# Kernel optimization log

Measured on AMD Instinct MI355X. Metric: run time of the kernel, lower is better.

The kernel has to match this reference:

```python
import jax, jax.numpy as jnp
import numpy as np

H = 64
FF = 128
V = 64
B = 256
L = 4096


def setup_inputs() -> dict:
    key = jax.random.key(0)
    ks = jax.random.split(key, 16)
    s = 0.02
    inp = {
        'seq':   jax.random.randint(ks[0], (B, L), 0, V, dtype=jnp.int32),
        'embed': jax.random.normal(ks[1], (V, H), jnp.float32) * s,
        'W1':    jax.random.normal(ks[2], (H, FF), jnp.float32) * s,
        'b1':    jnp.zeros((FF,), jnp.float32),
        'W2':    jax.random.normal(ks[3], (FF, H), jnp.float32) * s,
        'b2':    jnp.zeros((H,), jnp.float32),
        'gamma': jnp.ones((H,), jnp.float32),
        'beta':  jnp.zeros((H,), jnp.float32),
        'Wk':    jax.random.normal(ks[4], (H, H), jnp.float32) * s,
        'Wv':    jax.random.normal(ks[5], (H, H), jnp.float32) * s,
        'Wq':    jax.random.normal(ks[6], (H, H), jnp.float32) * s,
        'Wr':    jax.random.normal(ks[7], (H, H), jnp.float32) * s,
        'br':    jnp.zeros((H,), jnp.float32),
        'Wo':    jax.random.normal(ks[8], (H, V), jnp.float32) * s,
        'bo':    jnp.zeros((V,), jnp.float32),
    }
    return inp


def reference(seq, embed, W1, b1, W2, b2, gamma, beta, Wk, Wv, Wq, Wr, br, Wo, bo):
    # token embedding + FFN residual + LayerNorm
    h = embed[seq]                                            # (B,L,H)
    x = h + jnp.maximum(h @ W1 + b1, 0.0) @ W2 + b2
    mu = x.mean(-1, keepdims=True)
    var = ((x - mu) ** 2).mean(-1, keepdims=True)
    hn = (x - mu) * jax.lax.rsqrt(var + 1e-5) * gamma + beta  # (B,L,H)

    # precompute all keys/values for steps 0..L-2 (batched GEMMs)
    hk = hn[:, :-1]                                           # (B,L-1,H)
    k = hk @ Wk
    v = hk @ Wv
    kn = k / jnp.maximum(jnp.linalg.norm(k, axis=-1, keepdims=True), 1e-12)

    # sequential delta-rule fast-weight update via scan over time
    def step(M, kv):
        kt, vt = kv                                           # (B,H), (B,H)
        vp = jnp.einsum('bij,bj->bi', M, kt)                  # predicted value
        M = M + jnp.einsum('bi,bj->bij', vt - vp, kt)         # rank-1 delta write
        return M, None

    M0 = jnp.zeros((hn.shape[0], H, H), hn.dtype)
    M, _ = jax.lax.scan(step, M0, (kn.transpose(1, 0, 2), v.transpose(1, 0, 2)))

    # read out with last-position query
    q = hn[:, -1] @ Wq                                        # (B,H)
    r = jnp.einsum('bij,bj->bi', M, q) @ Wr + br
    return r @ Wo + bo                                        # (B,V)
```

## Files before the change

### kernel.cpp

```cpp
#include <hip/hip_runtime.h>
#include <hip/hip_bf16.h>

#define H_ 64
#define FF_ 128
#define V_ 64
#define B_ 256
#define L_ 4096

typedef __attribute__((ext_vector_type(2))) float f32x2;
typedef __attribute__((ext_vector_type(4))) int i32x4;

__device__ __forceinline__ float wsum64(float x) {
  #pragma unroll
  for (int m = 32; m; m >>= 1) x += __shfl_xor(x, m, 64);
  return x;
}
__device__ __forceinline__ float readlane_f(float x, int lane) {
  return __int_as_float(__builtin_amdgcn_readlane(__float_as_int(x), lane));
}

__global__ __launch_bounds__(64) void build_tables(
    const float* __restrict__ embed, const float* __restrict__ W1,
    const float* __restrict__ b1, const float* __restrict__ W2,
    const float* __restrict__ b2, const float* __restrict__ gamma,
    const float* __restrict__ beta, const float* __restrict__ Wk,
    const float* __restrict__ Wv, const float* __restrict__ Wq,
    float2* __restrict__ kv_table, float* __restrict__ q_table)
{
  const int tok = blockIdx.x;
  const int l = threadIdx.x;
  __shared__ float sh_h[H_];
  __shared__ float sh_a[FF_];
  __shared__ float sh_n[H_];

  float h = embed[tok * H_ + l];
  sh_h[l] = h;
  __syncthreads();

  float a0 = b1[l], a1 = b1[l + 64];
  #pragma unroll 8
  for (int j = 0; j < H_; ++j) {
    float hj = sh_h[j];
    a0 = fmaf(hj, W1[j * FF_ + l], a0);
    a1 = fmaf(hj, W1[j * FF_ + l + 64], a1);
  }
  sh_a[l]      = fmaxf(a0, 0.f);
  sh_a[l + 64] = fmaxf(a1, 0.f);
  __syncthreads();

  float x = h + b2[l];
  #pragma unroll 8
  for (int f = 0; f < FF_; ++f) x = fmaf(sh_a[f], W2[f * H_ + l], x);

  float mu = wsum64(x) * (1.0f / 64.0f);
  float d = x - mu;
  float var = wsum64(d * d) * (1.0f / 64.0f);
  float hn = d * rsqrtf(var + 1e-5f) * gamma[l] + beta[l];
  sh_n[l] = hn;
  __syncthreads();

  float k = 0.f, v = 0.f, q = 0.f;
  #pragma unroll 8
  for (int i = 0; i < H_; ++i) {
    float hi = sh_n[i];
    k = fmaf(hi, Wk[i * H_ + l], k);
    v = fmaf(hi, Wv[i * H_ + l], v);
    q = fmaf(hi, Wq[i * H_ + l], q);
  }
  float n2 = wsum64(k * k);
  float kn = k / fmaxf(sqrtf(n2), 1e-12f);
  kv_table[tok * H_ + l] = make_float2(kn, v);
  q_table[tok * H_ + l] = q;
}

__global__ __launch_bounds__(64) void build_gram(
    const float2* __restrict__ kv_table, float* __restrict__ gram)
{
  const int arow = blockIdx.x;
  const int j = threadIdx.x;
  float s = 0.f;
  #pragma unroll 8
  for (int i = 0; i < H_; ++i)
    s = fmaf(kv_table[arow * H_ + i].x, kv_table[j * H_ + i].x, s);
  gram[arow * H_ + j] = s;
}

#define DS64(dst, addr)  asm volatile("ds_read_b64 %0, %1"  : "=v"(dst) : "v"(addr))
#define DS128(dst, addr) asm volatile("ds_read_b128 %0, %1" : "=v"(dst) : "v"(addr))
#define LGKM(n) do { asm volatile("s_waitcnt lgkmcnt(" #n ")" ::: "memory"); \
                     __builtin_amdgcn_sched_barrier(0); } while (0)

#define PREP(S) do { \
  ss##S##0 = __builtin_amdgcn_readfirstlane(tk##S.w); \
  ss##S##1 = __builtin_amdgcn_readfirstlane(tk##S.z); \
  ss##S##2 = __builtin_amdgcn_readfirstlane(tk##S.y); \
  ss##S##3 = __builtin_amdgcn_readfirstlane(tk##S.x); \
  DS64(rb##S##0, gv_base + (unsigned)(ss##S##0) * 512u); \
  DS64(rb##S##1, gv_base + (unsigned)(ss##S##1) * 512u); \
  DS64(rb##S##2, gv_base + (unsigned)(ss##S##2) * 512u); \
  DS64(rb##S##3, gv_base + (unsigned)(ss##S##3) * 512u); \
} while (0)

#define TOKLD(S) do { \
  DS128(tk##S, atok); \
  atok = (atok >= tok_base + 16u) ? (atok - 16u) : tok_base; \
} while (0)

#define EXEC(S) do { \
  float d_; \
  d_ = readlane_f(a, ss##S##0); a = fmaf(-d_, (rb##S##0).x, a); r = fmaf(d_, (rb##S##0).y, r); \
  d_ = readlane_f(a, ss##S##1); a = fmaf(-d_, (rb##S##1).x, a); r = fmaf(d_, (rb##S##1).y, r); \
  d_ = readlane_f(a, ss##S##2); a = fmaf(-d_, (rb##S##2).x, a); r = fmaf(d_, (rb##S##2).y, r); \
  d_ = readlane_f(a, ss##S##3); a = fmaf(-d_, (rb##S##3).x, a); r = fmaf(d_, (rb##S##3).y, r); \
} while (0)

#define PHASE(EP, PP) do { \
  LGKM(5); \
  PREP(PP); \
  TOKLD(EP); \
  LGKM(11); \
  EXEC(EP); \
} while (0)

__global__ __launch_bounds__(64) void scan_kernel(
    const int* __restrict__ seq, const float2* __restrict__ kv_table,
    const float* __restrict__ q_table, const float* __restrict__ gram,
    const float* __restrict__ Wr, const float* __restrict__ br,
    const float* __restrict__ Wo, const float* __restrict__ bo,
    float* __restrict__ out)
{
  const int b = blockIdx.x, l = threadIdx.x;
  __shared__ __align__(16) int stok[L_];
  __shared__ float kn_s[64 * 65];
  __shared__ __align__(8) float2 gv_s[64 * 64];
  __shared__ float qs[64], sh_r[64], sh_rr[64];

  {
    const int4* src = reinterpret_cast<const int4*>(seq + b * L_);
    int4* dst = reinterpret_cast<int4*>(stok);
    for (int i = l; i < 1024; i += 64) dst[i] = src[i];
  }
  for (int idx = l * 2; idx < 4096; idx += 128) {
    float4 kv2 = *reinterpret_cast<const float4*>(&kv_table[idx]);
    float2 g2 = *reinterpret_cast<const float2*>(&gram[idx]);
    int row = idx >> 6, col = idx & 63;
    kn_s[row * 65 + col] = kv2.x;
    kn_s[row * 65 + col + 1] = kv2.z;
    gv_s[idx] = make_float2(g2.x, kv2.y);
    gv_s[idx + 1] = make_float2(g2.y, kv2.w);
  }
  __syncthreads();

  const int tq = stok[L_ - 1];
  qs[l] = q_table[tq * 64 + l];
  __syncthreads();

  float a = 0.f;
  #pragma unroll 8
  for (int i = 0; i < 64; ++i) a = fmaf(kn_s[l * 65 + i], qs[i], a);
  float r = 0.f;

  const float2* gvl = gv_s + l;
  #pragma unroll
  for (int t = 4094; t >= 4092; --t) {
    int s0 = __builtin_amdgcn_readfirstlane(stok[t]);
    float2 g = gvl[s0 * 64];
    float c0 = readlane_f(a, s0);
    a = fmaf(-c0, g.x, a);
    r = fmaf(c0, g.y, r);
  }

  unsigned tok_base = (unsigned)(size_t)stok;
  unsigned gv_base  = (unsigned)(size_t)gv_s + (unsigned)l * 8u;
  i32x4 tk0, tk1, tk2, tk3;
  f32x2 rb00, rb01, rb02, rb03, rb10, rb11, rb12, rb13,
        rb20, rb21, rb22, rb23, rb30, rb31, rb32, rb33;
  int ss00, ss01, ss02, ss03, ss10, ss11, ss12, ss13,
      ss20, ss21, ss22, ss23, ss30, ss31, ss32, ss33;

  DS128(tk0, tok_base + 16352u);
  DS128(tk1, tok_base + 16336u);
  LGKM(0);
  PREP(0);
  DS128(tk2, tok_base + 16320u);
  PREP(1);
  DS128(tk3, tok_base + 16304u);
  unsigned atok = tok_base + 16288u;

  #pragma unroll 1
  for (int it = 0; it < 255; ++it) {
    PHASE(0, 2);
    PHASE(1, 3);
    PHASE(2, 0);
    PHASE(3, 1);
  }
  PHASE(0, 2);
  PHASE(1, 3);
  PHASE(2, 0);
  LGKM(0);

  sh_r[l] = r;
  __syncthreads();
  float rr = br[l];
  #pragma unroll 8
  for (int i = 0; i < 64; ++i) rr = fmaf(sh_r[i], Wr[i * 64 + l], rr);
  sh_rr[l] = rr;
  __syncthreads();
  float o = bo[l];
  #pragma unroll 8
  for (int j = 0; j < 64; ++j) o = fmaf(sh_rr[j], Wo[j * 64 + l], o);
  out[b * V_ + l] = o;
}

extern "C" void kernel_launch(void* const* d_in, const int* in_sizes, int n_in,
                              void* d_out, int out_size, void* d_ws, size_t ws_size,
                              hipStream_t stream) {
  const int*   seq   = (const int*)  d_in[0];
  const float* embed = (const float*)d_in[1];
  const float* W1    = (const float*)d_in[2];
  const float* b1    = (const float*)d_in[3];
  const float* W2    = (const float*)d_in[4];
  const float* b2    = (const float*)d_in[5];
  const float* gamma = (const float*)d_in[6];
  const float* beta  = (const float*)d_in[7];
  const float* Wk    = (const float*)d_in[8];
  const float* Wv    = (const float*)d_in[9];
  const float* Wq    = (const float*)d_in[10];
  const float* Wr    = (const float*)d_in[11];
  const float* br    = (const float*)d_in[12];
  const float* Wo    = (const float*)d_in[13];
  const float* bo    = (const float*)d_in[14];
  float* out = (float*)d_out;

  float2* kv_table = (float2*)d_ws;
  float*  q_table  = (float*)((char*)d_ws + 32 * 1024);
  float*  gram     = (float*)((char*)d_ws + 48 * 1024);

  build_tables<<<V_, 64, 0, stream>>>(embed, W1, b1, W2, b2, gamma, beta,
                                      Wk, Wv, Wq, kv_table, q_table);
  build_gram<<<V_, 64, 0, stream>>>(kv_table, gram);
  scan_kernel<<<B_, 64, 0, stream>>>(seq, kv_table, q_table, gram,
                                     Wr, br, Wo, bo, out);
}
```

Before: 204.7 us.

## Precompute per-4-step correction coefficients to break serial readlane chain in scan

```diff
diff --git a/kernel.cpp b/kernel.cpp
--- a/kernel.cpp
+++ b/kernel.cpp
@@ -90,36 +90,59 @@
 #define LGKM(n) do { asm volatile("s_waitcnt lgkmcnt(" #n ")" ::: "memory"); \
                      __builtin_amdgcn_sched_barrier(0); } while (0)
 
-#define PREP(S) do { \
-  ss##S##0 = __builtin_amdgcn_readfirstlane(tk##S.w); \
-  ss##S##1 = __builtin_amdgcn_readfirstlane(tk##S.z); \
-  ss##S##2 = __builtin_amdgcn_readfirstlane(tk##S.y); \
-  ss##S##3 = __builtin_amdgcn_readfirstlane(tk##S.x); \
-  DS64(rb##S##0, gv_base + (unsigned)(ss##S##0) * 512u); \
-  DS64(rb##S##1, gv_base + (unsigned)(ss##S##1) * 512u); \
-  DS64(rb##S##2, gv_base + (unsigned)(ss##S##2) * 512u); \
-  DS64(rb##S##3, gv_base + (unsigned)(ss##S##3) * 512u); \
-} while (0)
-
-#define TOKLD(S) do { \
-  DS128(tk##S, atok); \
-  atok = (atok >= tok_base + 16u) ? (atok - 16u) : tok_base; \
+#define PREP_DS(S) do { \
+  unsigned pk = (unsigned)(rc##S.x); \
+  DS64(rb##S##0, gv_base + (pk & 63u) * 512u); \
+  DS64(rb##S##1, gv_base + ((pk >> 6) & 63u) * 512u); \
+  DS64(rb##S##2, gv_base + ((pk >> 12) & 63u) * 512u); \
+  DS64(rb##S##3, gv_base + ((pk >> 18) & 63u) * 512u); \
+} while (0)
+
+#define RECLD(S) do { \
+  unsigned ar_ = (arec > rec_max) ? rec_max : arec; \
+  DS128(rc##S, ar_); \
+  DS128(rm##S, ar_ + 16u); \
+  arec += 32u; \
+} while (0)
+
+#define PREP_SEL(S) do { \
+  int ps_ = __builtin_amdgcn_readfirstlane(rc##S.x); \
+  sl##S##0 = ps_ & 63; \
+  sl##S##1 = (ps_ >> 6) & 63; \
+  sl##S##2 = (ps_ >> 12) & 63; \
+  sl##S##3 = (ps_ >> 18) & 63; \
 } while (0)
 
 #define EXEC(S) do { \
-  float d_; \
-  d_ = readlane_f(a, ss##S##0); a = fmaf(-d_, (rb##S##0).x, a); r = fmaf(d_, (rb##S##0).y, r); \
-  d_ = readlane_f(a, ss##S##1); a = fmaf(-d_, (rb##S##1).x, a); r = fmaf(d_, (rb##S##1).y, r); \
-  d_ = readlane_f(a, ss##S##2); a = fmaf(-d_, (rb##S##2).x, a); r = fmaf(d_, (rb##S##2).y, r); \
-  d_ = readlane_f(a, ss##S##3); a = fmaf(-d_, (rb##S##3).x, a); r = fmaf(d_, (rb##S##3).y, r); \
-} while (0)
-
-#define PHASE(EP, PP) do { \
-  LGKM(5); \
-  PREP(PP); \
-  TOKLD(EP); \
-  LGKM(11); \
-  EXEC(EP); \
+  float d0 = readlane_f(a, sl##S##0); \
+  float d1 = readlane_f(a, sl##S##1); \
+  float d2 = readlane_f(a, sl##S##2); \
+  float d3 = readlane_f(a, sl##S##3); \
+  float m10 = __int_as_float(rc##S.y); \
+  float m20 = __int_as_float(rc##S.z); \
+  float m21 = __int_as_float(rc##S.w); \
+  float m30 = __int_as_float(rm##S.x); \
+  float m31 = __int_as_float(rm##S.y); \
+  float m32 = __int_as_float(rm##S.z); \
+  float c0 = d0; \
+  float c1 = fmaf(m10, d0, d1); \
+  float c2 = fmaf(m20, d0, fmaf(m21, d1, d2)); \
+  float c3 = fmaf(m30, d0, fmaf(m31, d1, fmaf(m32, d2, d3))); \
+  float p01_ = fmaf(c1, (rb##S##1).x, c0 * (rb##S##0).x); \
+  float p23_ = fmaf(c3, (rb##S##3).x, c2 * (rb##S##2).x); \
+  a = a - p01_ - p23_; \
+  r = fmaf(c0, (rb##S##0).y, r); \
+  r = fmaf(c1, (rb##S##1).y, r); \
+  r = fmaf(c2, (rb##S##2).y, r); \
+  r = fmaf(c3, (rb##S##3).y, r); \
+} while (0)
+
+#define PHASE(E, P2) do { \
+  LGKM(6); \
+  PREP_DS(P2); \
+  EXEC(E); \
+  RECLD(E); \
+  PREP_SEL(P2); \
 } while (0)
 
 __global__ __launch_bounds__(64) void scan_kernel(
@@ -130,16 +153,11 @@
     float* __restrict__ out)
 {
   const int b = blockIdx.x, l = threadIdx.x;
-  __shared__ __align__(16) int stok[L_];
   __shared__ float kn_s[64 * 65];
-  __shared__ __align__(8) float2 gv_s[64 * 64];
+  __shared__ __align__(16) float2 gv_s[64 * 64];
+  __shared__ __align__(16) int rec_s[1023 * 8];
   __shared__ float qs[64], sh_r[64], sh_rr[64];
 
-  {
-    const int4* src = reinterpret_cast<const int4*>(seq + b * L_);
-    int4* dst = reinterpret_cast<int4*>(stok);
-    for (int i = l; i < 1024; i += 64) dst[i] = src[i];
-  }
   for (int idx = l * 2; idx < 4096; idx += 128) {
     float4 kv2 = *reinterpret_cast<const float4*>(&kv_table[idx]);
     float2 g2 = *reinterpret_cast<const float2*>(&gram[idx]);
@@ -151,7 +169,34 @@
   }
   __syncthreads();
 
-  const int tq = stok[L_ - 1];
+  for (int rcd = l; rcd < 1023; rcd += 64) {
+    const int4 tv = *reinterpret_cast<const int4*>(seq + b * L_ + (4088 - 4 * rcd));
+    int s0 = tv.w, s1 = tv.z, s2 = tv.y, s3 = tv.x;
+    float g10 = gv_s[s0 * 64 + s1].x;
+    float g20 = gv_s[s0 * 64 + s2].x;
+    float g21 = gv_s[s1 * 64 + s2].x;
+    float g30 = gv_s[s0 * 64 + s3].x;
+    float g31 = gv_s[s1 * 64 + s3].x;
+    float g32 = gv_s[s2 * 64 + s3].x;
+    float m10 = -g10;
+    float m21 = -g21;
+    float m20 = -g20 - g21 * m10;
+    float m32 = -g32;
+    float m31 = -g31 - g32 * m21;
+    float m30 = -g30 - g31 * m10 - g32 * m20;
+    int* rp = rec_s + rcd * 8;
+    rp[0] = s0 | (s1 << 6) | (s2 << 12) | (s3 << 18);
+    rp[1] = __float_as_int(m10);
+    rp[2] = __float_as_int(m20);
+    rp[3] = __float_as_int(m21);
+    rp[4] = __float_as_int(m30);
+    rp[5] = __float_as_int(m31);
+    rp[6] = __float_as_int(m32);
+    rp[7] = 0;
+  }
+  __syncthreads();
+
+  const int tq = seq[b * L_ + 4095];
   qs[l] = q_table[tq * 64 + l];
   __syncthreads();
 
@@ -163,29 +208,32 @@
   const float2* gvl = gv_s + l;
   #pragma unroll
   for (int t = 4094; t >= 4092; --t) {
-    int s0 = __builtin_amdgcn_readfirstlane(stok[t]);
+    int s0 = seq[b * L_ + t];
     float2 g = gvl[s0 * 64];
     float c0 = readlane_f(a, s0);
     a = fmaf(-c0, g.x, a);
     r = fmaf(c0, g.y, r);
   }
 
-  unsigned tok_base = (unsigned)(size_t)stok;
   unsigned gv_base  = (unsigned)(size_t)gv_s + (unsigned)l * 8u;
-  i32x4 tk0, tk1, tk2, tk3;
+  unsigned rec_base = (unsigned)(size_t)rec_s;
+  unsigned rec_max  = rec_base + 32u * 1022u;
+  unsigned arec = rec_base;
+  i32x4 rc0, rc1, rc2, rc3, rm0, rm1, rm2, rm3;
   f32x2 rb00, rb01, rb02, rb03, rb10, rb11, rb12, rb13,
         rb20, rb21, rb22, rb23, rb30, rb31, rb32, rb33;
-  int ss00, ss01, ss02, ss03, ss10, ss11, ss12, ss13,
-      ss20, ss21, ss22, ss23, ss30, ss31, ss32, ss33;
-
-  DS128(tk0, tok_base + 16352u);
-  DS128(tk1, tok_base + 16336u);
+  int sl00, sl01, sl02, sl03, sl10, sl11, sl12, sl13,
+      sl20, sl21, sl22, sl23, sl30, sl31, sl32, sl33;
+
+  RECLD(0);
+  RECLD(1);
   LGKM(0);
-  PREP(0);
-  DS128(tk2, tok_base + 16320u);
-  PREP(1);
-  DS128(tk3, tok_base + 16304u);
-  unsigned atok = tok_base + 16288u;
+  PREP_DS(0);
+  RECLD(2);
+  PREP_DS(1);
+  RECLD(3);
+  PREP_SEL(0);
+  PREP_SEL(1);
 
   #pragma unroll 1
   for (int it = 0; it < 255; ++it) {
```

Result: slower. 219.7 us (+7.3%).
